# Performance work log

Hardware: AMD Instinct MI355X
Metric: run time of the kernel (lower is better)

Reference implementation:

```python
import jax, jax.numpy as jnp
import numpy as np

B, T, D = 4, 2048, 1024
EPS = 1e-5


def _layernorm(x, g, b):
    mu = jnp.mean(x, axis=-1, keepdims=True)
    var = jnp.var(x, axis=-1, keepdims=True)
    return (x - mu) * jax.lax.rsqrt(var + EPS) * g + b


def setup_inputs() -> dict:
    key = jax.random.key(0)
    ks = jax.random.split(key, 16)
    s = lambda fan_in: 1.0 / np.sqrt(fan_in)
    return {
        "x": jax.random.normal(ks[0], (B, T, D), dtype=jnp.float32),
        "ln1_g": jnp.ones((D,), jnp.float32),
        "ln1_b": jnp.zeros((D,), jnp.float32),
        "Wqkv": jax.random.uniform(ks[1], (D, 3 * D), jnp.float32, -s(D), s(D)),
        "bqkv": jnp.zeros((3 * D,), jnp.float32),
        "Wproj": jax.random.uniform(ks[2], (D, D), jnp.float32, -s(D), s(D)),
        "bproj": jnp.zeros((D,), jnp.float32),
        "ln2_g": jnp.ones((D,), jnp.float32),
        "ln2_b": jnp.zeros((D,), jnp.float32),
        "W1": jax.random.uniform(ks[3], (D, 4 * D), jnp.float32, -s(D), s(D)),
        "b1": jnp.zeros((4 * D,), jnp.float32),
        "W2": jax.random.uniform(ks[4], (4 * D, D), jnp.float32, -s(4 * D), s(4 * D)),
        "b2": jnp.zeros((D,), jnp.float32),
    }


def reference(x, ln1_g, ln1_b, Wqkv, bqkv, Wproj, bproj, ln2_g, ln2_b, W1, b1, W2, b2):
    # NOTE: no residual connections in the original Block.
    h = _layernorm(x, ln1_g, ln1_b)
    kqv = h @ Wqkv + bqkv                      # [B,T,3D]
    k, q, v = jnp.split(kqv, 3, axis=-1)       # split order: k, q, v
    # Original scales by 1/sqrt(k.size(-1)) AFTER transposing k -> 1/sqrt(T).
    scores = jnp.einsum("btd,bsd->bts", q, k) * (1.0 / np.sqrt(T))
    causal = jnp.tril(jnp.ones((T, T), dtype=bool))
    scores = jnp.where(causal, scores, -jnp.inf)
    attn = jax.nn.softmax(scores, axis=-1)
    a = jnp.einsum("bts,bsd->btd", attn, v)
    a = a @ Wproj + bproj
    h2 = _layernorm(a, ln2_g, ln2_b)
    m = jax.nn.gelu(h2 @ W1 + b1, approximate=True)
    return m @ W2 + b2
```

## Files before the change

### kernel.cpp

```cpp
#include <hip/hip_runtime.h>
#include <hip/hip_bf16.h>

typedef __hip_bfloat16 bf16;
typedef __bf16 bf16x8 __attribute__((ext_vector_type(8)));
typedef __bf16 bf16x4 __attribute__((ext_vector_type(4)));
typedef __bf16 bf16x2 __attribute__((ext_vector_type(2)));
typedef float f32x4 __attribute__((ext_vector_type(4)));

static constexpr int Bq = 4, Tq = 2048, Dq = 1024;

__device__ inline float b2f(bf16 h) { return __bfloat162float(h); }
__device__ inline bf16 f2b(float f) { return __float2bfloat16(f); }

__device__ __forceinline__ void gload_lds16(const bf16* g, bf16* lds_wave_base) {
    __builtin_amdgcn_global_load_lds((const __attribute__((address_space(1))) void*)g,
                                     (__attribute__((address_space(3))) void*)lds_wave_base,
                                     16, 0, 0);
}

__device__ __forceinline__ float fast_gelu(float x) {
    float u = x * (0.7978845608028654f + 0.03567740814183427f * x * x);
    float e = __builtin_amdgcn_exp2f(-2.885390081777927f * u);
    return x * __builtin_amdgcn_rcpf(1.f + e);
}

__device__ inline void ld4f(const float* p, float* v) {
    float4 t = *reinterpret_cast<const float4*>(p);
    v[0] = t.x; v[1] = t.y; v[2] = t.z; v[3] = t.w;
}
__device__ inline void ld4f(const bf16* p, float* v) {
    bf16x4 t = *reinterpret_cast<const bf16x4*>(p);
    v[0] = (float)t[0]; v[1] = (float)t[1]; v[2] = (float)t[2]; v[3] = (float)t[3];
}

template <typename Tin>
__device__ __forceinline__ void ln_body(const Tin* __restrict__ x, const float* __restrict__ g,
                                        const float* __restrict__ b, bf16* __restrict__ out,
                                        int row, float* sred)
{
    const int tid = threadIdx.x;
    const int s0 = tid * 4;
    const Tin* xr = x + (size_t)row * Dq;
    bf16* orow = out + (size_t)row * Dq;
    float v[4], gv[4], bv[4];
    ld4f(xr + s0, v);
    ld4f(g + s0, gv);
    ld4f(b + s0, bv);
    float sum = v[0] + v[1] + v[2] + v[3];
    float sq = v[0]*v[0] + v[1]*v[1] + v[2]*v[2] + v[3]*v[3];
    for (int o = 32; o > 0; o >>= 1) { sum += __shfl_xor(sum, o); sq += __shfl_xor(sq, o); }
    const int w = tid >> 6;
    if ((tid & 63) == 0) { sred[w] = sum; sred[4 + w] = sq; }
    __syncthreads();
    const float ts = sred[0] + sred[1] + sred[2] + sred[3];
    const float tq = sred[4] + sred[5] + sred[6] + sred[7];
    const float mean = ts / Dq;
    const float rs = rsqrtf(tq / Dq - mean * mean + 1e-5f);
    bf16x4 o4;
    #pragma unroll
    for (int i = 0; i < 4; ++i) o4[i] = (__bf16)((v[i] - mean) * rs * gv[i] + bv[i]);
    *reinterpret_cast<bf16x4*>(orow + s0) = o4;
}

__global__ void ln_kernel(const bf16* __restrict__ x, const float* __restrict__ g,
                          const float* __restrict__ b, bf16* __restrict__ out)
{
    __shared__ float sred[8];
    ln_body(x, g, b, out, blockIdx.x, sred);
}

__global__ void prep_kernel(const float* __restrict__ x, const float* __restrict__ g,
                            const float* __restrict__ b, bf16* __restrict__ h,
                            const float* __restrict__ Wqkv, bf16* __restrict__ WqkvT,
                            const float* __restrict__ Wproj, bf16* __restrict__ WprojT,
                            const float* __restrict__ W1, bf16* __restrict__ W1T,
                            const float* __restrict__ W2, bf16* __restrict__ W2T)
{
    __shared__ float smem[64 * 65];
    int id = blockIdx.x;
    if (id < 8192) { ln_body(x, g, b, h, id, smem); return; }
    id -= 8192;
    const float* src; bf16* dst; long ldin, ldout; int gx;
    if (id < 768)       { src = Wqkv;  dst = WqkvT;  ldin = 3072; ldout = 1024; gx = 48; }
    else if (id < 1024) { id -= 768;  src = Wproj; dst = WprojT; ldin = 1024; ldout = 1024; gx = 16; }
    else if (id < 2048) { id -= 1024; src = W1;    dst = W1T;    ldin = 4096; ldout = 1024; gx = 64; }
    else                { id -= 2048; src = W2;    dst = W2T;    ldin = 1024; ldout = 4096; gx = 16; }
    const int c0 = (id % gx) * 64, r0 = (id / gx) * 64;
    const int tid = threadIdx.x;
    const int tx = tid & 63, ty = tid >> 6;
    float (*tile)[65] = reinterpret_cast<float(*)[65]>(smem);
    #pragma unroll
    for (int i = 0; i < 16; ++i) {
        int r = ty + i * 4;
        tile[r][tx] = src[(size_t)(r0 + r) * ldin + c0 + tx];
    }
    __syncthreads();
    const int px = tid & 31, cy = tid >> 5;
    #pragma unroll
    for (int i = 0; i < 8; ++i) {
        int cc = cy + i * 8;
        bf16x2 p;
        p[0] = (__bf16)tile[px * 2][cc];
        p[1] = (__bf16)tile[px * 2 + 1][cc];
        *reinterpret_cast<bf16x2*>(&dst[(size_t)(c0 + cc) * ldout + r0 + px * 2]) = p;
    }
}

template <int ACT, int TRI, int CK, int FR>
__global__ void gemm128(const bf16* __restrict__ A, const bf16* __restrict__ Bt,
                        const float* __restrict__ bias,
                        bf16* __restrict__ Cb, float* __restrict__ Cf,
                        int K, long lda, long ldb, long ldc,
                        long sA, long sB, long sC, float scale,
                        const bf16* __restrict__ vsrc, bf16* __restrict__ vdst)
{
    __shared__ bf16 As[128 * 64];
    __shared__ bf16 Bs[128 * 64];

    int bx, by;
    if (TRI) {
        const int lin = blockIdx.x;
        if (lin >= 136) {
            const int idx = lin - 136;
            const int c0 = (idx & 15) * 64, r0 = (idx >> 4) * 64;
            const bf16* ip = vsrc + (size_t)blockIdx.z * ((size_t)Tq * 3072);
            bf16* op = vdst + (size_t)blockIdx.z * ((size_t)Dq * Tq);
            bf16 (*tile)[66] = reinterpret_cast<bf16(*)[66]>(As);
            const int tid = threadIdx.x;
            const int tx = tid & 31, ty = tid >> 5;
            #pragma unroll
            for (int i = 0; i < 8; ++i) {
                int r = ty + i * 8;
                *reinterpret_cast<bf16x2*>(&tile[r][tx * 2]) =
                    *reinterpret_cast<const bf16x2*>(&ip[(size_t)(r0 + r) * 3072 + c0 + tx * 2]);
            }
            __syncthreads();
            #pragma unroll
            for (int i = 0; i < 8; ++i) {
                int cc = ty + i * 8;
                bf16x2 p;
                p[0] = tile[tx * 2][cc];
                p[1] = tile[tx * 2 + 1][cc];
                *reinterpret_cast<bf16x2*>(&op[(size_t)(c0 + cc) * 2048 + r0 + tx * 2]) = p;
            }
            return;
        }
        int t = (int)((sqrtf(8.f * lin + 1.f) - 1.f) * 0.5f);
        while ((t + 1) * (t + 2) / 2 <= lin) ++t;
        while (t * (t + 1) / 2 > lin) --t;
        by = t; bx = lin - t * (t + 1) / 2;
    } else {
        const int gx = gridDim.x, gy = gridDim.y;
        const int lin = blockIdx.x + gx * blockIdx.y;
        const int band = lin & 7;
        const int idx = lin >> 3;
        bx = idx % gx;
        by = band * (gy >> 3) + idx / gx;
    }

    const int m0 = by * 128, n0 = bx * 128;
    const int Kend = CK ? min(K, m0 + 128) : K;

    const bf16* Ab = A + (size_t)blockIdx.z * sA;
    const bf16* Bb = Bt + (size_t)blockIdx.z * sB;
    const int tid = threadIdx.x;
    const int wid = tid >> 6, lane = tid & 63;
    const int wr = wid >> 1, wc = wid & 1;
    const int l15 = lane & 15, quad = lane >> 4;

    const int rloc = lane >> 3, slot = lane & 7;
    const bf16* agp = Ab + (size_t)(m0 + wid * 32 + rloc) * lda + (slot ^ rloc) * 8;
    const bf16* bgp = Bb + (size_t)(n0 + wid * 32 + rloc) * ldb + (slot ^ rloc) * 8;
    bf16* awb = As + wid * 32 * 64;
    bf16* bwb = Bs + wid * 32 * 64;

    const int afo = (wr * 64 + l15) * 64 + ((quad ^ (l15 & 7)) * 8);
    const int bfo = (wc * 64 + l15) * 64 + ((quad ^ (l15 & 7)) * 8);

    f32x4 acc[4][4];
    #pragma unroll
    for (int i = 0; i < 4; ++i)
        #pragma unroll
        for (int j = 0; j < 4; ++j) acc[i][j] = (f32x4){0.f, 0.f, 0.f, 0.f};

    f32x4 acc_l[4];
    bf16x8 ones;
    if (FR) {
        #pragma unroll
        for (int i = 0; i < 4; ++i) acc_l[i] = (f32x4){0.f, 0.f, 0.f, 0.f};
        #pragma unroll
        for (int i = 0; i < 8; ++i) ones[i] = (__bf16)1.0f;
    }

    for (int k0 = 0; k0 < Kend; k0 += 64) {
        #pragma unroll
        for (int i = 0; i < 4; ++i) {
            gload_lds16(agp + k0 + (size_t)(i * 8) * lda, awb + i * 8 * 64);
            gload_lds16(bgp + k0 + (size_t)(i * 8) * ldb, bwb + i * 8 * 64);
        }
        __syncthreads();

        bf16x8 af0[4], bf0[4], af1[4], bf1[4];
        #pragma unroll
        for (int i = 0; i < 4; ++i) {
            af0[i] = *reinterpret_cast<const bf16x8*>(As + (afo ^ 0)  + i * 1024);
            af1[i] = *reinterpret_cast<const bf16x8*>(As + (afo ^ 32) + i * 1024);
        }
        #pragma unroll
        for (int j = 0; j < 4; ++j) {
            bf0[j] = *reinterpret_cast<const bf16x8*>(Bs + (bfo ^ 0)  + j * 1024);
            bf1[j] = *reinterpret_cast<const bf16x8*>(Bs + (bfo ^ 32) + j * 1024);
        }
        #pragma unroll
        for (int i = 0; i < 4; ++i)
            #pragma unroll
            for (int j = 0; j < 4; ++j)
                acc[i][j] = __builtin_amdgcn_mfma_f32_16x16x32_bf16(af0[i], bf0[j], acc[i][j], 0, 0, 0);
        if (FR) {
            #pragma unroll
            for (int i = 0; i < 4; ++i)
                acc_l[i] = __builtin_amdgcn_mfma_f32_16x16x32_bf16(af0[i], ones, acc_l[i], 0, 0, 0);
        }
        #pragma unroll
        for (int i = 0; i < 4; ++i)
            #pragma unroll
            for (int j = 0; j < 4; ++j)
                acc[i][j] = __builtin_amdgcn_mfma_f32_16x16x32_bf16(af1[i], bf1[j], acc[i][j], 0, 0, 0);
        if (FR) {
            #pragma unroll
            for (int i = 0; i < 4; ++i)
                acc_l[i] = __builtin_amdgcn_mfma_f32_16x16x32_bf16(af1[i], ones, acc_l[i], 0, 0, 0);
        }

        __syncthreads();
    }

    #pragma unroll
    for (int i = 0; i < 4; ++i) {
        const int row = m0 + wr * 64 + i * 16 + quad * 4;
        #pragma unroll
        for (int j = 0; j < 4; ++j) {
            const int col = n0 + wc * 64 + j * 16 + l15;
            const float bv = bias ? bias[col] : 0.f;
            #pragma unroll
            for (int r = 0; r < 4; ++r) {
                float vv = scale * acc[i][j][r] + bv;
                if (ACT == 1) vv = fast_gelu(vv);
                else if (ACT == 2)
                    vv = (col <= row + r) ? __builtin_amdgcn_exp2f(1.4426950408889634f * vv) : 0.f;
                if (FR) vv *= __builtin_amdgcn_rcpf(acc_l[i][r]);
                const size_t idx2 = (size_t)(row + r) * ldc + col + (size_t)blockIdx.z * sC;
                if (Cf) Cf[idx2] = vv;
                else    Cb[idx2] = f2b(vv);
            }
        }
    }
}

extern "C" void kernel_launch(void* const* d_in, const int* in_sizes, int n_in,
                              void* d_out, int out_size, void* d_ws, size_t ws_size,
                              hipStream_t stream)
{
    (void)in_sizes; (void)n_in; (void)out_size; (void)ws_size;
    const float* x     = (const float*)d_in[0];
    const float* ln1g  = (const float*)d_in[1];
    const float* ln1b  = (const float*)d_in[2];
    const float* Wqkv  = (const float*)d_in[3];
    const float* bqkv  = (const float*)d_in[4];
    const float* Wproj = (const float*)d_in[5];
    const float* bproj = (const float*)d_in[6];
    const float* ln2g  = (const float*)d_in[7];
    const float* ln2b  = (const float*)d_in[8];
    const float* W1    = (const float*)d_in[9];
    const float* b1    = (const float*)d_in[10];
    const float* W2    = (const float*)d_in[11];
    const float* b2    = (const float*)d_in[12];
    float* out = (float*)d_out;

    char* ws = (char*)d_ws;
    size_t off = 0;
    auto alloc = [&](size_t elems) { bf16* p = (bf16*)(ws + off); off += elems * sizeof(bf16); return p; };
    bf16* WqkvT  = alloc(3072UL * 1024);
    bf16* WprojT = alloc(1024UL * 1024);
    bf16* W1T    = alloc(4096UL * 1024);
    bf16* W2T    = alloc(1024UL * 4096);
    bf16* h      = alloc(8192UL * 1024);
    bf16* kqv    = alloc(8192UL * 3072);
    bf16* vT     = alloc(4UL * 1024 * 2048);
    bf16* attn   = alloc(4UL * 2048 * 2048);
    bf16* a   = h;
    bf16* p   = kqv;
    bf16* h2  = kqv + 8192UL * 1024;
    bf16* m   = kqv + 2UL * 8192 * 1024;

    const long T3D = (long)Tq * 3072, TT = (long)Tq * Tq, DT = (long)Dq * Tq, TD = (long)Tq * Dq;

    prep_kernel<<<11264, 256, 0, stream>>>(x, ln1g, ln1b, h,
                                           Wqkv, WqkvT, Wproj, WprojT, W1, W1T, W2, W2T);

    gemm128<0,0,0,0><<<dim3(24, 64, 1), 256, 0, stream>>>(h, WqkvT, bqkv, kqv, nullptr,
        1024, 1024L, 1024L, 3072L, 0L, 0L, 0L, 1.f, nullptr, nullptr);

    gemm128<2,1,0,0><<<dim3(648, 1, 4), 256, 0, stream>>>(kqv + 1024, kqv, nullptr, attn, nullptr,
        1024, 3072L, 3072L, 2048L, T3D, T3D, TT, 0.022097086912079608f, kqv + 2048, vT);

    gemm128<0,0,1,1><<<dim3(8, 16, 4), 256, 0, stream>>>(attn, vT, nullptr, a, nullptr,
        2048, 2048L, 2048L, 1024L, TT, DT, TD, 1.f, nullptr, nullptr);

    gemm128<0,0,0,0><<<dim3(8, 64, 1), 256, 0, stream>>>(a, WprojT, bproj, p, nullptr,
        1024, 1024L, 1024L, 1024L, 0L, 0L, 0L, 1.f, nullptr, nullptr);

    ln_kernel<<<8192, 256, 0, stream>>>(p, ln2g, ln2b, h2);

    gemm128<1,0,0,0><<<dim3(32, 64, 1), 256, 0, stream>>>(h2, W1T, b1, m, nullptr,
        1024, 1024L, 1024L, 4096L, 0L, 0L, 0L, 1.f, nullptr, nullptr);

    gemm128<0,0,0,0><<<dim3(8, 64, 1), 256, 0, stream>>>(m, W2T, b2, nullptr, out,
        4096, 4096L, 4096L, 1024L, 0L, 0L, 0L, 1.f, nullptr, nullptr);
}
```

Before: 486.3 us.

## Add 256x256-tile 8-wave GEMM with phased LDS pipeline for QKV and MLP-up

Introduces a new gemm256 kernel with 256x256 output tiles, 512 threads, double-buffered LDS filled by direct global-to-LDS loads, and a four-phase schedule that interleaves LDS reads, next-tile prefetch and MFMA bursts. It uses grouped block swizzling into eight bands for L2 locality. The QKV projection and the first MLP GEMM (with GELU) now use it. Larger tiles raise arithmetic intensity and cut global traffic, but the kernel needs 128KB of LDS per block and has fewer blocks, which may limit occupancy and load balance on 256 CUs.

```diff
diff --git a/kernel.cpp b/kernel.cpp
--- a/kernel.cpp
+++ b/kernel.cpp
@@ -257,6 +257,133 @@
     }
 }
 
+template <int ACT>
+__global__ __launch_bounds__(512, 2) void gemm256(
+        const bf16* __restrict__ A, const bf16* __restrict__ Bt,
+        const float* __restrict__ bias, bf16* __restrict__ C,
+        int K, long lda, long ldb, long ldc)
+{
+    __shared__ bf16 As[2][256 * 64];
+    __shared__ bf16 Bs[2][256 * 64];
+
+    const int gx = gridDim.x, gy = gridDim.y;
+    const int lin = blockIdx.x + gx * blockIdx.y;
+    const int band = lin & 7;
+    const int idx = lin >> 3;
+    const int bx = idx % gx;
+    const int by = band * (gy >> 3) + idx / gx;
+    const int m0 = by * 256, n0 = bx * 256;
+
+    const int tid = threadIdx.x;
+    const int wid = tid >> 6, lane = tid & 63;
+    const int wr = wid >> 2, wc = wid & 3;
+    const int l15 = lane & 15, quad = lane >> 4;
+    const int rloc = lane >> 3, slot = lane & 7;
+
+    const bf16* agp = A + (size_t)(m0 + wid * 8 + rloc) * lda + (slot ^ rloc) * 8;
+    const bf16* bgp = Bt + (size_t)(n0 + wid * 8 + rloc) * ldb + (slot ^ rloc) * 8;
+
+    auto issueA = [&](int buf, int t2, int R) {
+        gload_lds16(agp + (size_t)R * lda + t2 * 64, &As[buf][(R + wid * 8) * 64]);
+    };
+    auto issueB = [&](int buf, int t2, int R) {
+        gload_lds16(bgp + (size_t)R * ldb + t2 * 64, &Bs[buf][(R + wid * 8) * 64]);
+    };
+
+    const int xg = (quad ^ (l15 & 7)) * 8;
+    const int afo = (wr * 128 + l15) * 64 + xg;
+    const int bfo = (wc * 64 + l15) * 64 + xg;
+
+    f32x4 acc[8][4];
+    #pragma unroll
+    for (int i = 0; i < 8; ++i)
+        #pragma unroll
+        for (int j = 0; j < 4; ++j) acc[i][j] = (f32x4){0.f, 0.f, 0.f, 0.f};
+
+    const int nt = K >> 6;
+
+    issueA(0, 0, 0); issueA(0, 0, 128);
+    issueB(0, 0, 0); issueB(0, 0, 128); issueB(0, 0, 64); issueB(0, 0, 192);
+    issueA(0, 0, 64); issueA(0, 0, 192);
+    asm volatile("s_waitcnt vmcnt(2)" ::: "memory");
+    __builtin_amdgcn_s_barrier();
+
+#define PH_READS(p, rh, ks)                                                              \
+    {   const int xr = (ks) << 5;                                                        \
+        _Pragma("unroll")                                                                \
+        for (int i = 0; i < 4; ++i)                                                      \
+            a[i] = *reinterpret_cast<const bf16x8*>(&As[p][(afo + ((rh)*4 + i) * 1024) ^ xr]); \
+        _Pragma("unroll")                                                                \
+        for (int j = 0; j < 4; ++j)                                                      \
+            b[j] = *reinterpret_cast<const bf16x8*>(&Bs[p][(bfo + (j) * 1024) ^ xr]);    \
+    }
+#define PH_MFMA(rh)                                                                      \
+    {   __builtin_amdgcn_s_setprio(1);                                                   \
+        _Pragma("unroll")                                                                \
+        for (int i = 0; i < 4; ++i)                                                      \
+            _Pragma("unroll")                                                            \
+            for (int j = 0; j < 4; ++j)                                                  \
+                acc[(rh)*4 + i][j] =                                                     \
+                    __builtin_amdgcn_mfma_f32_16x16x32_bf16(a[i], b[j], acc[(rh)*4 + i][j], 0, 0, 0); \
+        __builtin_amdgcn_s_setprio(0);                                                   \
+    }
+#define BAR()   __builtin_amdgcn_s_barrier()
+#define LGKM0() asm volatile("s_waitcnt lgkmcnt(0)" ::: "memory")
+
+    for (int t = 0; t < nt; ++t) {
+        const int p = t & 1, q = p ^ 1, tn = t + 1;
+        const bool pre = tn < nt;
+        bf16x8 a[4], b[4];
+
+        PH_READS(p, 0, 0);
+        if (pre) { issueA(q, tn, 0); issueA(q, tn, 128); issueB(q, tn, 0); }
+        BAR(); LGKM0();
+        PH_MFMA(0);
+        BAR();
+
+        PH_READS(p, 0, 1);
+        if (pre) { issueB(q, tn, 128); issueB(q, tn, 64); issueB(q, tn, 192); }
+        BAR(); LGKM0();
+        PH_MFMA(0);
+        if (pre) asm volatile("s_waitcnt vmcnt(6)" ::: "memory");
+        else     asm volatile("s_waitcnt vmcnt(0)" ::: "memory");
+        BAR();
+
+        PH_READS(p, 1, 0);
+        BAR(); LGKM0();
+        PH_MFMA(1);
+        BAR();
+
+        PH_READS(p, 1, 1);
+        if (pre) { issueA(q, tn, 64); issueA(q, tn, 192); }
+        BAR(); LGKM0();
+        PH_MFMA(1);
+        if (pre) asm volatile("s_waitcnt vmcnt(2)" ::: "memory");
+        else     asm volatile("s_waitcnt vmcnt(0)" ::: "memory");
+        BAR();
+    }
+#undef PH_READS
+#undef PH_MFMA
+#undef BAR
+#undef LGKM0
+
+    #pragma unroll
+    for (int i = 0; i < 8; ++i) {
+        const int row = m0 + wr * 128 + i * 16 + quad * 4;
+        #pragma unroll
+        for (int j = 0; j < 4; ++j) {
+            const int col = n0 + wc * 64 + j * 16 + l15;
+            const float bv = bias ? bias[col] : 0.f;
+            #pragma unroll
+            for (int r = 0; r < 4; ++r) {
+                float vv = acc[i][j][r] + bv;
+                if (ACT == 1) vv = fast_gelu(vv);
+                C[(size_t)(row + r) * ldc + col] = f2b(vv);
+            }
+        }
+    }
+}
+
 extern "C" void kernel_launch(void* const* d_in, const int* in_sizes, int n_in,
                               void* d_out, int out_size, void* d_ws, size_t ws_size,
                               hipStream_t stream)
@@ -298,8 +425,8 @@
     prep_kernel<<<11264, 256, 0, stream>>>(x, ln1g, ln1b, h,
                                            Wqkv, WqkvT, Wproj, WprojT, W1, W1T, W2, W2T);
 
-    gemm128<0,0,0,0><<<dim3(24, 64, 1), 256, 0, stream>>>(h, WqkvT, bqkv, kqv, nullptr,
-        1024, 1024L, 1024L, 3072L, 0L, 0L, 0L, 1.f, nullptr, nullptr);
+    gemm256<0><<<dim3(12, 32, 1), 512, 0, stream>>>(h, WqkvT, bqkv, kqv,
+        1024, 1024L, 1024L, 3072L);
 
     gemm128<2,1,0,0><<<dim3(648, 1, 4), 256, 0, stream>>>(kqv + 1024, kqv, nullptr, attn, nullptr,
         1024, 3072L, 3072L, 2048L, T3D, T3D, TT, 0.022097086912079608f, kqv + 2048, vT);
@@ -312,8 +439,8 @@
 
     ln_kernel<<<8192, 256, 0, stream>>>(p, ln2g, ln2b, h2);
 
-    gemm128<1,0,0,0><<<dim3(32, 64, 1), 256, 0, stream>>>(h2, W1T, b1, m, nullptr,
-        1024, 1024L, 1024L, 4096L, 0L, 0L, 0L, 1.f, nullptr, nullptr);
+    gemm256<1><<<dim3(16, 32, 1), 512, 0, stream>>>(h2, W1T, b1, m,
+        1024, 1024L, 1024L, 4096L);
 
     gemm128<0,0,0,0><<<dim3(8, 64, 1), 256, 0, stream>>>(m, W2T, b2, nullptr, out,
         4096, 4096L, 4096L, 1024L, 0L, 0L, 0L, 1.f, nullptr, nullptr);
```

Measured after the change: 493.3 us. Within noise of the previous version (+1.4%).
